# Performance work log

Measured on AMD Instinct MI355X. Metric: run time of the kernel, lower is better.

## Reference

```python
import jax, jax.numpy as jnp
import numpy as np
from jax.scipy.linalg import block_diag

N_STATE, N_INPUT, HORIZON = 32, 16, 64


def setup_inputs() -> dict:
    key = jax.random.key(0)
    kA, kB, kC, kx = jax.random.split(key, 4)
    n_all = N_STATE + N_INPUT
    A = jax.random.normal(kA, (N_STATE, N_STATE), dtype=jnp.float32)
    B = jax.random.normal(kB, (N_STATE, N_INPUT), dtype=jnp.float32)
    Craw = jax.random.normal(kC, (HORIZON, n_all, n_all), dtype=jnp.float32)
    # symmetric positive-definite stage costs -> nonsingular KKT system
    C = jnp.einsum('tij,tkj->tik', Craw, Craw) / jnp.sqrt(jnp.float32(n_all)) \
        + jnp.eye(n_all, dtype=jnp.float32)
    x0 = jax.random.normal(kx, (N_STATE,), dtype=jnp.float32)
    return {"A": A, "B": B, "C": C, "T": HORIZON, "x0": x0}


def reference(A, B, C, T, x0):
    n_state = A.shape[0]
    n_input = B.shape[1]
    n_all = n_state + n_input
    dt = A.dtype

    # cost_mat: block-diagonal [n_all*T, n_all*T]
    cost_mat = block_diag(*C)

    # dynamics: [n_state*T, n_all*T]
    AB = jnp.concatenate((A, B), axis=1)              # [n_state, n_all]
    AB_blk = block_diag(*([AB] * (T - 1)))            # [(T-1)*n_state, (T-1)*n_all]
    dynamics = jnp.zeros((n_state * T, n_all * T), dtype=dt)
    dynamics = dynamics.at[:n_state, :n_state].set(jnp.eye(n_state, dtype=dt))
    dynamics = dynamics.at[n_state:n_state + (T - 1) * n_state,
                           :(T - 1) * n_all].set(AB_blk)
    # -I coupling entries: row n_state*t + i, col n_all*t + i, t=1..T-1
    t = jnp.arange(1, T)
    rows = (n_state * t)[:, None] + jnp.arange(n_state)[None, :]
    cols = (n_all * t)[:, None] + jnp.arange(n_state)[None, :]
    dynamics = dynamics.at[rows, cols].set(jnp.asarray(-1.0, dt))

    zero_mat = jnp.zeros((n_state * T, n_state * T), dtype=dt)
    full_mat = jnp.block([[cost_mat, dynamics.T],
                          [dynamics, zero_mat]])      # [(n_all+n_state)*T]^2

    # rhs: zeros except x0 at the start of the dynamics block
    sol = jnp.zeros(n_all * T + n_state * T, dtype=dt)
    sol = sol.at[n_all * T: n_all * T + n_state].set(x0)

    tau_mu = jnp.linalg.solve(full_mat, sol[:, None])[:, 0]
    tau_star = tau_mu[:n_all * T]
    mu_star = tau_mu[n_all * T:]
    return tau_star, mu_star
```

## Files before the change

kernel.cpp:

```cpp
#include <hip/hip_runtime.h>


namespace {

constexpr int NS  = 32;
constexpr int NI  = 16;
constexpr int NA  = 48;
constexpr int TT  = 64;
constexpr int NTH = 256;

__device__ __forceinline__ void fma4(float4& a, float s, const float4& b) {
  a.x += s * b.x; a.y += s * b.y; a.z += s * b.z; a.w += s * b.w;
}
__device__ __forceinline__ void fms4(float4& a, float s, const float4& b) {
  a.x -= s * b.x; a.y -= s * b.y; a.z -= s * b.z; a.w -= s * b.w;
}
__device__ __forceinline__ float dot4(const float4& a, const float4& b) {
  return a.x * b.x + a.y * b.y + a.z * b.z + a.w * b.w;
}
__device__ __forceinline__ float rdlane(float v, int l) {
  return __int_as_float(__builtin_amdgcn_readlane(__float_as_int(v), l));
}

template<int K>
__device__ __forceinline__ void tile_outer(const float* Acol0, int lda,
                                           const float* Bcol0, int ldb,
                                           float4 acc[4]) {
  #pragma unroll
  for (int m = 0; m < K; ++m) {
    const float4 va = *(const float4*)(Acol0 + m * lda);
    const float4 vb = *(const float4*)(Bcol0 + m * ldb);
    fma4(acc[0], va.x, vb); fma4(acc[1], va.y, vb);
    fma4(acc[2], va.z, vb); fma4(acc[3], va.w, vb);
  }
}

template<int KQ>
__device__ __forceinline__ void tile_dot(const float* Arow0, int lda,
                                         const float* Brow0, int ldb,
                                         float acc[4][4]) {
  #pragma unroll
  for (int q = 0; q < KQ; ++q) {
    float4 va[4], vb[4];
    #pragma unroll
    for (int r = 0; r < 4; ++r) va[r] = *(const float4*)(Arow0 + r * lda + 4 * q);
    #pragma unroll
    for (int c = 0; c < 4; ++c) vb[c] = *(const float4*)(Brow0 + c * ldb + 4 * q);
    #pragma unroll
    for (int r = 0; r < 4; ++r)
      #pragma unroll
      for (int c = 0; c < 4; ++c) acc[r][c] += dot4(va[r], vb[c]);
  }
}

__global__ __launch_bounds__(NTH, 1) void init_elems(
    const float* __restrict__ A, const float* __restrict__ Bm,
    const float* __restrict__ C, float* __restrict__ S0) {
  __shared__ float sC [NA][NA];
  __shared__ float sAB[NS][NA];
  __shared__ float sRi[NI][NI];
  __shared__ float sRiST[NS][NI];
  __shared__ float sBRi [NS][NI];
  const int t = blockIdx.x, tid = threadIdx.x, lane = tid & 63, wid = tid >> 6;
  const float* Ct = C + (size_t)t * NA * NA;

  for (int e = tid; e < NA * NA; e += NTH) sC[e / NA][e % NA] = Ct[e];
  for (int e = tid; e < NS * NA; e += NTH) {
    int i = e / NA, j = e % NA;
    sAB[i][j] = (j < NS) ? A[i * NS + j] : Bm[i * NI + (j - NS)];
  }
  __syncthreads();

  if (wid == 0 && lane < 32) {
    const int c = lane;
    float f[NI];
    #pragma unroll
    for (int i = 0; i < NI; ++i)
      f[i] = (c < NI) ? sC[NS + i][NS + c] : ((c - NI) == i ? 1.f : 0.f);
    #pragma unroll
    for (int k = 0; k < NI; ++k) {
      float mi[NI];
      #pragma unroll
      for (int i = 0; i < NI; ++i) mi[i] = rdlane(f[i], k);
      const float inv = 1.0f / mi[k];
      f[k] *= inv;
      #pragma unroll
      for (int i = 0; i < NI; ++i) if (i != k) f[i] -= mi[i] * f[k];
    }
    if (c >= NI) {
      #pragma unroll
      for (int i = 0; i < NI; ++i) sRi[i][c - NI] = f[i];
    }
  }
  __syncthreads();

  if (tid < 32) {
    const int a = tid >> 2, b = tid & 3;
    float acc[4][4];
    #pragma unroll
    for (int r = 0; r < 4; ++r)
      #pragma unroll
      for (int c = 0; c < 4; ++c) acc[r][c] = 0.f;
    tile_dot<4>(&sC[4 * a][NS], NA, &sRi[4 * b][0], NI, acc);
    #pragma unroll
    for (int r = 0; r < 4; ++r)
      *(float4*)&sRiST[4 * a + r][4 * b] =
          make_float4(acc[r][0], acc[r][1], acc[r][2], acc[r][3]);
  } else if (tid < 64) {
    const int q = tid - 32, a = q >> 2, b = q & 3;
    float acc[4][4];
    #pragma unroll
    for (int r = 0; r < 4; ++r)
      #pragma unroll
      for (int c = 0; c < 4; ++c) acc[r][c] = 0.f;
    tile_dot<4>(&sAB[4 * a][NS], NA, &sRi[4 * b][0], NI, acc);
    #pragma unroll
    for (int r = 0; r < 4; ++r)
      *(float4*)&sBRi[4 * a + r][4 * b] =
          make_float4(acc[r][0], acc[r][1], acc[r][2], acc[r][3]);
  }
  __syncthreads();

  float* outA = S0 + (size_t)t * 3072;
  float* outC = outA + 1024;
  float* outJ = outA + 2048;
  if (tid < 64) {
    const int a = tid >> 3, b = tid & 7;
    float acc[4][4];
    #pragma unroll
    for (int r = 0; r < 4; ++r)
      #pragma unroll
      for (int c = 0; c < 4; ++c) acc[r][c] = 0.f;
    tile_dot<4>(&sRiST[4 * a][0], NI, &sC[4 * b][NS], NA, acc);
    #pragma unroll
    for (int r = 0; r < 4; ++r) {
      const float4 q4 = *(const float4*)&sC[4 * a + r][4 * b];
      *(float4*)(outJ + (4 * a + r) * NS + 4 * b) =
          make_float4(q4.x - acc[r][0], q4.y - acc[r][1],
                      q4.z - acc[r][2], q4.w - acc[r][3]);
    }
  } else if (tid < 128) {
    const int q = tid - 64, a = q >> 3, b = q & 7;
    float acc[4][4];
    #pragma unroll
    for (int r = 0; r < 4; ++r)
      #pragma unroll
      for (int c = 0; c < 4; ++c) acc[r][c] = 0.f;
    tile_dot<4>(&sBRi[4 * a][0], NI, &sC[4 * b][NS], NA, acc);
    #pragma unroll
    for (int r = 0; r < 4; ++r) {
      const float4 a4 = *(const float4*)&sAB[4 * a + r][4 * b];
      *(float4*)(outA + (4 * a + r) * NS + 4 * b) =
          make_float4(a4.x - acc[r][0], a4.y - acc[r][1],
                      a4.z - acc[r][2], a4.w - acc[r][3]);
    }
  } else if (tid < 192) {
    const int q = tid - 128, a = q >> 3, b = q & 7;
    float acc[4][4];
    #pragma unroll
    for (int r = 0; r < 4; ++r)
      #pragma unroll
      for (int c = 0; c < 4; ++c) acc[r][c] = 0.f;
    tile_dot<4>(&sBRi[4 * a][0], NI, &sAB[4 * b][NS], NA, acc);
    #pragma unroll
    for (int r = 0; r < 4; ++r)
      *(float4*)(outC + (4 * a + r) * NS + 4 * b) =
          make_float4(acc[r][0], acc[r][1], acc[r][2], acc[r][3]);
  }
}

__global__ __launch_bounds__(NTH, 1) void scan_level(
    const float* __restrict__ Sin, float* __restrict__ Sout, int off) {
  const int t = blockIdx.x, tid = threadIdx.x, lane = tid & 63, wid = tid >> 6;
  const float* Ei = Sin + (size_t)t * 3072;
  float* Eo = Sout + (size_t)t * 3072;
  if (t + off >= TT) {
    const float4* src = (const float4*)Ei;
    float4* dst = (float4*)Eo;
    #pragma unroll
    for (int r = 0; r < 3; ++r) dst[tid + 256 * r] = src[tid + 256 * r];
    return;
  }
  const float* Ej = Sin + (size_t)(t + off) * 3072;

  __shared__ float sAi[NS][NS], sCi[NS][NS], sJi[NS][NS];
  __shared__ float sAj[NS][NS], sCj[NS][NS], sJj[NS][NS];
  __shared__ float sAjT[NS][NS];
  __shared__ float sT1[NS][NS], sT1T[NS][NS];
  __shared__ float sY1[NS][NS], sY2[NS][NS], sY3T[NS][NS], sW[NS][NS];
  __shared__ float sX[NS][NS], sZ[NS][NS];

  {
    const float4* a4 = (const float4*)Ei;
    ((float4*)sAi)[tid] = a4[tid];
    ((float4*)sCi)[tid] = a4[256 + tid];
    ((float4*)sJi)[tid] = a4[512 + tid];
    const float4* b4 = (const float4*)Ej;
    ((float4*)sAj)[tid] = b4[tid];
    ((float4*)sCj)[tid] = b4[256 + tid];
    ((float4*)sJj)[tid] = b4[512 + tid];
  }
  __syncthreads();
  #pragma unroll
  for (int r = 0; r < 4; ++r) {
    const int e = tid + 256 * r, i = e >> 5, j = e & 31;
    sAjT[j][i] = sAj[i][j];
  }
  if (tid < 64) {
    const int a = tid >> 3, b = tid & 7;
    float4 acc[4] = {make_float4(0,0,0,0), make_float4(0,0,0,0),
                     make_float4(0,0,0,0), make_float4(0,0,0,0)};
    tile_outer<NS>(&sCi[0][4 * a], NS, &sJj[0][4 * b], NS, acc);
    if (a == b) { acc[0].x += 1.f; acc[1].y += 1.f; acc[2].z += 1.f; acc[3].w += 1.f; }
    #pragma unroll
    for (int r = 0; r < 4; ++r) *(float4*)&sX[4 * a + r][4 * b] = acc[r];
  }
  __syncthreads();
  if (wid == 0) {
    const int c = lane;
    float f[NS];
    #pragma unroll
    for (int i = 0; i < NS; ++i)
      f[i] = (c < NS) ? sX[i][c] : ((c - NS) == i ? 1.f : 0.f);
    #pragma unroll
    for (int k = 0; k < NS; ++k) {
      float mi[NS];
      #pragma unroll
      for (int i = 0; i < NS; ++i) mi[i] = rdlane(f[i], k);
      const float inv = 1.0f / mi[k];
      f[k] *= inv;
      #pragma unroll
      for (int i = 0; i < NS; ++i) if (i != k) f[i] -= mi[i] * f[k];
    }
    if (c >= NS) {
      const int col = c - NS;
      #pragma unroll
      for (int i = 0; i < NS; ++i) sT1[i][col] = f[i];
      #pragma unroll
      for (int q = 0; q < 8; ++q)
        *(float4*)&sT1T[col][4 * q] =
            make_float4(f[4 * q], f[4 * q + 1], f[4 * q + 2], f[4 * q + 3]);
    }
  }
  __syncthreads();
  if (tid < 192) {
    const int grp = tid >> 6, q = tid & 63, a = q >> 3, b = q & 7;
    float4 acc[4] = {make_float4(0,0,0,0), make_float4(0,0,0,0),
                     make_float4(0,0,0,0), make_float4(0,0,0,0)};
    if (grp == 0) {
      tile_outer<NS>(&sT1T[0][4 * a], NS, &sAi[0][4 * b], NS, acc);
      #pragma unroll
      for (int r = 0; r < 4; ++r) *(float4*)&sY1[4 * a + r][4 * b] = acc[r];
    } else if (grp == 1) {
      tile_outer<NS>(&sT1T[0][4 * a], NS, &sCi[0][4 * b], NS, acc);
      #pragma unroll
      for (int r = 0; r < 4; ++r) *(float4*)&sY2[4 * a + r][4 * b] = acc[r];
    } else {
      tile_outer<NS>(&sT1[0][4 * a], NS, &sJj[0][4 * b], NS, acc);
      #pragma unroll
      for (int r = 0; r < 4; ++r) *(float4*)&sY3T[4 * a + r][4 * b] = acc[r];
    }
  }
  __syncthreads();
  if (tid < 192) {
    const int grp = tid >> 6, q = tid & 63, a = q >> 3, b = q & 7;
    float4 acc[4] = {make_float4(0,0,0,0), make_float4(0,0,0,0),
                     make_float4(0,0,0,0), make_float4(0,0,0,0)};
    if (grp == 0) {
      tile_outer<NS>(&sAjT[0][4 * a], NS, &sY1[0][4 * b], NS, acc);
      #pragma unroll
      for (int r = 0; r < 4; ++r) *(float4*)&sX[4 * a + r][4 * b] = acc[r];
    } else if (grp == 1) {
      tile_outer<NS>(&sAjT[0][4 * a], NS, &sY2[0][4 * b], NS, acc);
      #pragma unroll
      for (int r = 0; r < 4; ++r) *(float4*)&sZ[4 * a + r][4 * b] = acc[r];
    } else {
      tile_outer<NS>(&sY3T[0][4 * a], NS, &sAi[0][4 * b], NS, acc);
      #pragma unroll
      for (int r = 0; r < 4; ++r) *(float4*)&sW[4 * a + r][4 * b] = acc[r];
    }
  }
  __syncthreads();
  if (tid < 64) {
    const int a = tid >> 3, b = tid & 7;
    float acc[4][4];
    #pragma unroll
    for (int r = 0; r < 4; ++r)
      #pragma unroll
      for (int c = 0; c < 4; ++c) acc[r][c] = 0.f;
    tile_dot<8>(&sZ[4 * a][0], NS, &sAj[4 * b][0], NS, acc);
    #pragma unroll
    for (int r = 0; r < 4; ++r) {
      const float4 c4 = *(const float4*)&sCj[4 * a + r][4 * b];
      *(float4*)&sY2[4 * a + r][4 * b] =
          make_float4(acc[r][0] + c4.x, acc[r][1] + c4.y,
                      acc[r][2] + c4.z, acc[r][3] + c4.w);
    }
  } else if (tid < 128) {
    const int q = tid - 64, a = q >> 3, b = q & 7;
    float4 acc[4] = {make_float4(0,0,0,0), make_float4(0,0,0,0),
                     make_float4(0,0,0,0), make_float4(0,0,0,0)};
    tile_outer<NS>(&sAi[0][4 * a], NS, &sW[0][4 * b], NS, acc);
    #pragma unroll
    for (int r = 0; r < 4; ++r) {
      const float4 j4 = *(const float4*)&sJi[4 * a + r][4 * b];
      acc[r].x += j4.x; acc[r].y += j4.y; acc[r].z += j4.z; acc[r].w += j4.w;
      *(float4*)&sY1[4 * a + r][4 * b] = acc[r];
    }
  }
  __syncthreads();
  {
    float4* o = (float4*)Eo;
    o[tid]       = ((const float4*)sX)[tid];
    o[256 + tid] = ((const float4*)sY2)[tid];
    o[512 + tid] = ((const float4*)sY1)[tid];
  }
}

__global__ __launch_bounds__(NTH, 1) void kmat(
    const float* __restrict__ Sfin, const float* __restrict__ A,
    const float* __restrict__ Bm, const float* __restrict__ C,
    float* __restrict__ Kall, float* __restrict__ Mall) {
  __shared__ float sAB[NS][NA];
  __shared__ float sP [NS][NS];
  __shared__ float sG [NS][NA];
  __shared__ float sFu[NI][NA];
  __shared__ float sK [NI][NS];
  const int t = blockIdx.x, tid = threadIdx.x, lane = tid & 63, wid = tid >> 6;

  for (int e = tid; e < NS * NA; e += NTH) {
    int i = e / NA, j = e % NA;
    sAB[i][j] = (j < NS) ? A[i * NS + j] : Bm[i * NI + (j - NS)];
  }
  if (t == TT - 1) {
    ((float4*)sP)[tid] = make_float4(0.f, 0.f, 0.f, 0.f);
  } else {
    const float4* j4 = (const float4*)(Sfin + (size_t)(t + 1) * 3072 + 2048);
    ((float4*)sP)[tid] = j4[tid];
  }
  const int ui = tid / 12, uk = tid - 12 * ui;
  float4 cr0 = make_float4(0,0,0,0), cr1 = make_float4(0,0,0,0);
  float4 cr2 = make_float4(0,0,0,0), cr3 = make_float4(0,0,0,0);
  if (tid < 48) {
    const float* Ct = C + (size_t)t * NA * NA;
    cr0 = *(const float4*)&Ct[(NS + 4 * ui + 0) * NA + 4 * uk];
    cr1 = *(const float4*)&Ct[(NS + 4 * ui + 1) * NA + 4 * uk];
    cr2 = *(const float4*)&Ct[(NS + 4 * ui + 2) * NA + 4 * uk];
    cr3 = *(const float4*)&Ct[(NS + 4 * ui + 3) * NA + 4 * uk];
  }
  __syncthreads();
  if (tid < 96) {
    const int gi = tid / 12, gk = tid - 12 * gi;
    float4 acc[4] = {make_float4(0,0,0,0), make_float4(0,0,0,0),
                     make_float4(0,0,0,0), make_float4(0,0,0,0)};
    tile_outer<NS>(&sP[0][4 * gi], NS, &sAB[0][4 * gk], NA, acc);
    #pragma unroll
    for (int r = 0; r < 4; ++r) *(float4*)&sG[4 * gi + r][4 * gk] = acc[r];
  }
  __syncthreads();
  if (tid < 48) {
    float4 acc[4] = {cr0, cr1, cr2, cr3};
    tile_outer<NS>(&sAB[0][NS + 4 * ui], NA, &sG[0][4 * uk], NA, acc);
    #pragma unroll
    for (int r = 0; r < 4; ++r) *(float4*)&sFu[4 * ui + r][4 * uk] = acc[r];
  }
  __syncthreads();
  if (wid == 0) {
    const int col = (lane < 16) ? (NS + lane) : (lane - 16);
    float f[NI];
    #pragma unroll
    for (int i = 0; i < NI; ++i) f[i] = sFu[i][col];
    #pragma unroll
    for (int k = 0; k < NI; ++k) {
      float mi[NI];
      #pragma unroll
      for (int i = 0; i < NI; ++i) mi[i] = rdlane(f[i], k);
      const float inv = 1.0f / mi[k];
      f[k] *= inv;
      #pragma unroll
      for (int i = 0; i < NI; ++i) if (i != k) f[i] -= mi[i] * f[k];
    }
    if (lane >= 16 && lane < 48) {
      const int b = lane - 16;
      #pragma unroll
      for (int i = 0; i < NI; ++i) {
        sK[i][b] = f[i];
        Kall[(size_t)t * NI * NS + i * NS + b] = f[i];
      }
    }
  }
  __syncthreads();
  if (tid < 64) {
    const int ma = tid >> 3, mb = tid & 7;
    float4 a0 = *(const float4*)&sAB[4 * ma + 0][4 * mb];
    float4 a1 = *(const float4*)&sAB[4 * ma + 1][4 * mb];
    float4 a2 = *(const float4*)&sAB[4 * ma + 2][4 * mb];
    float4 a3 = *(const float4*)&sAB[4 * ma + 3][4 * mb];
    #pragma unroll
    for (int q = 0; q < 4; ++q) {
      const float4 vf0 = *(const float4*)&sAB[4 * ma + 0][NS + 4 * q];
      const float4 vf1 = *(const float4*)&sAB[4 * ma + 1][NS + 4 * q];
      const float4 vf2 = *(const float4*)&sAB[4 * ma + 2][NS + 4 * q];
      const float4 vf3 = *(const float4*)&sAB[4 * ma + 3][NS + 4 * q];
      #pragma unroll
      for (int d = 0; d < 4; ++d) {
        const float4 vkk = *(const float4*)&sK[4 * q + d][4 * mb];
        const float s0 = (d == 0) ? vf0.x : (d == 1) ? vf0.y : (d == 2) ? vf0.z : vf0.w;
        const float s1 = (d == 0) ? vf1.x : (d == 1) ? vf1.y : (d == 2) ? vf1.z : vf1.w;
        const float s2 = (d == 0) ? vf2.x : (d == 1) ? vf2.y : (d == 2) ? vf2.z : vf2.w;
        const float s3 = (d == 0) ? vf3.x : (d == 1) ? vf3.y : (d == 2) ? vf3.z : vf3.w;
        fms4(a0, s0, vkk); fms4(a1, s1, vkk); fms4(a2, s2, vkk); fms4(a3, s3, vkk);
      }
    }
    float4* Mt = (float4*)(Mall + (size_t)t * NS * NS);
    Mt[(4 * ma + 0) * 8 + mb] = a0;
    Mt[(4 * ma + 1) * 8 + mb] = a1;
    Mt[(4 * ma + 2) * 8 + mb] = a2;
    Mt[(4 * ma + 3) * 8 + mb] = a3;
  }
}

__global__ __launch_bounds__(NTH, 1) void finalize(
    const float* __restrict__ x0, const float* __restrict__ Sfin,
    const float* __restrict__ Kall, const float* __restrict__ Mall,
    float* __restrict__ out) {
  __shared__ float sZx[TT][NS];
  __shared__ float sMb[2 * NS * NS];
  const int tid = threadIdx.x, lane = tid & 63, wid = tid >> 6;

  if (wid == 0) {
    const float4* M4 = (const float4*)Mall;
    float4* sM4 = (float4*)sMb;
    if (lane < NS) { float v = x0[lane]; sZx[0][lane] = v; out[lane] = v; }
    float4 p0 = M4[lane], p1 = M4[64 + lane], p2 = M4[128 + lane], p3 = M4[192 + lane];
    asm volatile("s_waitcnt vmcnt(0)" ::: "memory");
    sM4[lane] = p0; sM4[64 + lane] = p1; sM4[128 + lane] = p2; sM4[192 + lane] = p3;
    asm volatile("s_waitcnt lgkmcnt(0)" ::: "memory");
    __builtin_amdgcn_sched_barrier(0);
    int cur = 0;
    for (int t = 0; t < TT - 1; ++t) {
      const bool pf = (t + 1 < TT - 1);
      if (pf) {
        const int b = (t + 1) * 256;
        p0 = M4[b + lane]; p1 = M4[b + 64 + lane];
        p2 = M4[b + 128 + lane]; p3 = M4[b + 192 + lane];
      }
      if (lane < NS) {
        const float4* xr = (const float4*)&sZx[t][0];
        const float4* mr = sM4 + cur * 256 + 8 * lane;
        float acc = 0.0f;
        #pragma unroll
        for (int q = 0; q < 8; ++q) acc += dot4(mr[q], xr[q]);
        sZx[t + 1][lane] = acc;
        out[(t + 1) * NA + lane] = acc;
      }
      if (pf) {
        asm volatile("s_waitcnt vmcnt(0)" ::: "memory");
        float4* d = sM4 + (cur ^ 1) * 256;
        d[lane] = p0; d[64 + lane] = p1; d[128 + lane] = p2; d[192 + lane] = p3;
      }
      asm volatile("s_waitcnt lgkmcnt(0)" ::: "memory");
      __builtin_amdgcn_sched_barrier(0);
      cur ^= 1;
    }
  }
  __syncthreads();

  const float4* K4 = (const float4*)Kall;
  #pragma unroll
  for (int rep = 0; rep < 4; ++rep) {
    const int idx = tid + 256 * rep;
    const int t = idx >> 4, i = idx & 15;
    const float4* xr = (const float4*)&sZx[t][0];
    float acc = 0.0f;
    #pragma unroll
    for (int q = 0; q < 8; ++q) acc += dot4(K4[(size_t)t * 128 + 8 * i + q], xr[q]);
    out[t * NA + NS + i] = -acc;
  }

  const float4* S4 = (const float4*)Sfin;
  for (int e = tid; e < TT * NS; e += NTH) {
    const int t = e >> 5, i = e & 31;
    const float4* xr = (const float4*)&sZx[t][0];
    float acc = 0.0f;
    #pragma unroll
    for (int q = 0; q < 8; ++q)
      acc += dot4(S4[(size_t)t * 768 + 512 + 8 * i + q], xr[q]);
    out[NA * TT + e] = (t == 0) ? -acc : acc;
  }
}

}

extern "C" void kernel_launch(void* const* d_in, const int* in_sizes, int n_in,
                              void* d_out, int out_size, void* d_ws, size_t ws_size,
                              hipStream_t stream) {
  const float* A  = (const float*)d_in[0];
  const float* Bm = (const float*)d_in[1];
  const float* C  = (const float*)d_in[2];
  const float* x0 = (const float*)d_in[4];
  float* out = (float*)d_out;

  float* Sb0  = (float*)d_ws;
  float* Sb1  = Sb0 + (size_t)TT * 3072;
  float* Kall = Sb1 + (size_t)TT * 3072;
  float* Mall = Kall + (size_t)TT * NI * NS;

  hipLaunchKernelGGL(init_elems, dim3(TT), dim3(NTH), 0, stream, A, Bm, C, Sb0);
  float* bufs[2] = {Sb0, Sb1};
  for (int l = 0; l < 6; ++l) {
    hipLaunchKernelGGL(scan_level, dim3(TT), dim3(NTH), 0, stream,
                       bufs[l & 1], bufs[(l + 1) & 1], 1 << l);
  }
  hipLaunchKernelGGL(kmat, dim3(TT), dim3(NTH), 0, stream,
                     Sb0, A, Bm, C, Kall, Mall);
  hipLaunchKernelGGL(finalize, dim3(1), dim3(NTH), 0, stream,
                     x0, Sb0, Kall, Mall, out);
}
```

Before: 138.0 us.

## Fuse all LQR stages into one persistent kernel with a software grid barrier

Merges the init, six scan levels, gain computation and finalize kernels into a single 64-block persistent kernel. Stages are separated by an atomic-counter grid barrier, which removes per-launch overhead between the many small dependent launches. The forward state rollout appears to be restructured, using cross-lane reads and a shared state buffer in workspace, and output is produced in parallel per block. It relies on all 64 blocks being co-resident and on the spin barrier being correct, and it adds a memset launch to reset the barrier counters.

```diff
diff --git a/kernel.cpp b/kernel.cpp
--- a/kernel.cpp
+++ b/kernel.cpp
@@ -8,6 +8,7 @@
 constexpr int NA  = 48;
 constexpr int TT  = 64;
 constexpr int NTH = 256;
+constexpr int NBLK = 64;
 
 __device__ __forceinline__ void fma4(float4& a, float s, const float4& b) {
   a.x += s * b.x; a.y += s * b.y; a.z += s * b.z; a.w += s * b.w;
@@ -53,440 +54,447 @@
   }
 }
 
-__global__ __launch_bounds__(NTH, 1) void init_elems(
+__device__ __forceinline__ void gbar(unsigned* cnt, unsigned* gen) {
+  __syncthreads();
+  if (threadIdx.x == 0) {
+    __threadfence();
+    const unsigned g = atomicAdd(gen, 0u);
+    const unsigned old = atomicAdd(cnt, 1u);
+    if (old == NBLK - 1) {
+      atomicExch(cnt, 0u);
+      __threadfence();
+      atomicAdd(gen, 1u);
+    } else {
+      while (atomicAdd(gen, 0u) == g) __builtin_amdgcn_s_sleep(2);
+    }
+    __threadfence();
+  }
+  __syncthreads();
+}
+
+__device__ __forceinline__ float step_dot(const float4 m[8], float x) {
+  float a0 = 0.f, a1 = 0.f, a2 = 0.f, a3 = 0.f;
+  #pragma unroll
+  for (int q = 0; q < 8; ++q) {
+    a0 += rdlane(x, 4 * q + 0) * m[q].x;
+    a1 += rdlane(x, 4 * q + 1) * m[q].y;
+    a2 += rdlane(x, 4 * q + 2) * m[q].z;
+    a3 += rdlane(x, 4 * q + 3) * m[q].w;
+  }
+  return (a0 + a1) + (a2 + a3);
+}
+
+__global__ __launch_bounds__(NTH, 1) void lqr_all(
     const float* __restrict__ A, const float* __restrict__ Bm,
-    const float* __restrict__ C, float* __restrict__ S0) {
+    const float* __restrict__ C, const float* __restrict__ x0,
+    float* __restrict__ out,
+    float* __restrict__ Sb0, float* __restrict__ Sb1,
+    float* __restrict__ Kall, float* __restrict__ Mall,
+    float* __restrict__ xs, unsigned* __restrict__ bar) {
   __shared__ float sC [NA][NA];
   __shared__ float sAB[NS][NA];
   __shared__ float sRi[NI][NI];
   __shared__ float sRiST[NS][NI];
   __shared__ float sBRi [NS][NI];
-  const int t = blockIdx.x, tid = threadIdx.x, lane = tid & 63, wid = tid >> 6;
-  const float* Ct = C + (size_t)t * NA * NA;
-
-  for (int e = tid; e < NA * NA; e += NTH) sC[e / NA][e % NA] = Ct[e];
-  for (int e = tid; e < NS * NA; e += NTH) {
-    int i = e / NA, j = e % NA;
-    sAB[i][j] = (j < NS) ? A[i * NS + j] : Bm[i * NI + (j - NS)];
-  }
-  __syncthreads();
-
-  if (wid == 0 && lane < 32) {
-    const int c = lane;
-    float f[NI];
-    #pragma unroll
-    for (int i = 0; i < NI; ++i)
-      f[i] = (c < NI) ? sC[NS + i][NS + c] : ((c - NI) == i ? 1.f : 0.f);
-    #pragma unroll
-    for (int k = 0; k < NI; ++k) {
-      float mi[NI];
-      #pragma unroll
-      for (int i = 0; i < NI; ++i) mi[i] = rdlane(f[i], k);
-      const float inv = 1.0f / mi[k];
-      f[k] *= inv;
-      #pragma unroll
-      for (int i = 0; i < NI; ++i) if (i != k) f[i] -= mi[i] * f[k];
-    }
-    if (c >= NI) {
-      #pragma unroll
-      for (int i = 0; i < NI; ++i) sRi[i][c - NI] = f[i];
-    }
-  }
-  __syncthreads();
-
-  if (tid < 32) {
-    const int a = tid >> 2, b = tid & 3;
-    float acc[4][4];
-    #pragma unroll
-    for (int r = 0; r < 4; ++r)
-      #pragma unroll
-      for (int c = 0; c < 4; ++c) acc[r][c] = 0.f;
-    tile_dot<4>(&sC[4 * a][NS], NA, &sRi[4 * b][0], NI, acc);
-    #pragma unroll
-    for (int r = 0; r < 4; ++r)
-      *(float4*)&sRiST[4 * a + r][4 * b] =
-          make_float4(acc[r][0], acc[r][1], acc[r][2], acc[r][3]);
-  } else if (tid < 64) {
-    const int q = tid - 32, a = q >> 2, b = q & 3;
-    float acc[4][4];
-    #pragma unroll
-    for (int r = 0; r < 4; ++r)
-      #pragma unroll
-      for (int c = 0; c < 4; ++c) acc[r][c] = 0.f;
-    tile_dot<4>(&sAB[4 * a][NS], NA, &sRi[4 * b][0], NI, acc);
-    #pragma unroll
-    for (int r = 0; r < 4; ++r)
-      *(float4*)&sBRi[4 * a + r][4 * b] =
-          make_float4(acc[r][0], acc[r][1], acc[r][2], acc[r][3]);
-  }
-  __syncthreads();
-
-  float* outA = S0 + (size_t)t * 3072;
-  float* outC = outA + 1024;
-  float* outJ = outA + 2048;
-  if (tid < 64) {
-    const int a = tid >> 3, b = tid & 7;
-    float acc[4][4];
-    #pragma unroll
-    for (int r = 0; r < 4; ++r)
-      #pragma unroll
-      for (int c = 0; c < 4; ++c) acc[r][c] = 0.f;
-    tile_dot<4>(&sRiST[4 * a][0], NI, &sC[4 * b][NS], NA, acc);
-    #pragma unroll
-    for (int r = 0; r < 4; ++r) {
-      const float4 q4 = *(const float4*)&sC[4 * a + r][4 * b];
-      *(float4*)(outJ + (4 * a + r) * NS + 4 * b) =
-          make_float4(q4.x - acc[r][0], q4.y - acc[r][1],
-                      q4.z - acc[r][2], q4.w - acc[r][3]);
-    }
-  } else if (tid < 128) {
-    const int q = tid - 64, a = q >> 3, b = q & 7;
-    float acc[4][4];
-    #pragma unroll
-    for (int r = 0; r < 4; ++r)
-      #pragma unroll
-      for (int c = 0; c < 4; ++c) acc[r][c] = 0.f;
-    tile_dot<4>(&sBRi[4 * a][0], NI, &sC[4 * b][NS], NA, acc);
-    #pragma unroll
-    for (int r = 0; r < 4; ++r) {
-      const float4 a4 = *(const float4*)&sAB[4 * a + r][4 * b];
-      *(float4*)(outA + (4 * a + r) * NS + 4 * b) =
-          make_float4(a4.x - acc[r][0], a4.y - acc[r][1],
-                      a4.z - acc[r][2], a4.w - acc[r][3]);
-    }
-  } else if (tid < 192) {
-    const int q = tid - 128, a = q >> 3, b = q & 7;
-    float acc[4][4];
-    #pragma unroll
-    for (int r = 0; r < 4; ++r)
-      #pragma unroll
-      for (int c = 0; c < 4; ++c) acc[r][c] = 0.f;
-    tile_dot<4>(&sBRi[4 * a][0], NI, &sAB[4 * b][NS], NA, acc);
-    #pragma unroll
-    for (int r = 0; r < 4; ++r)
-      *(float4*)(outC + (4 * a + r) * NS + 4 * b) =
-          make_float4(acc[r][0], acc[r][1], acc[r][2], acc[r][3]);
-  }
-}
-
-__global__ __launch_bounds__(NTH, 1) void scan_level(
-    const float* __restrict__ Sin, float* __restrict__ Sout, int off) {
-  const int t = blockIdx.x, tid = threadIdx.x, lane = tid & 63, wid = tid >> 6;
-  const float* Ei = Sin + (size_t)t * 3072;
-  float* Eo = Sout + (size_t)t * 3072;
-  if (t + off >= TT) {
-    const float4* src = (const float4*)Ei;
-    float4* dst = (float4*)Eo;
-    #pragma unroll
-    for (int r = 0; r < 3; ++r) dst[tid + 256 * r] = src[tid + 256 * r];
-    return;
-  }
-  const float* Ej = Sin + (size_t)(t + off) * 3072;
-
   __shared__ float sAi[NS][NS], sCi[NS][NS], sJi[NS][NS];
-  __shared__ float sAj[NS][NS], sCj[NS][NS], sJj[NS][NS];
-  __shared__ float sAjT[NS][NS];
+  __shared__ float sAj[NS][NS], sCj[NS][NS], sJj[NS][NS], sAjT[NS][NS];
   __shared__ float sT1[NS][NS], sT1T[NS][NS];
   __shared__ float sY1[NS][NS], sY2[NS][NS], sY3T[NS][NS], sW[NS][NS];
-  __shared__ float sX[NS][NS], sZ[NS][NS];
+  __shared__ float sX[NS][NS], sZm[NS][NS];
+  __shared__ float sP[NS][NS], sG[NS][NA], sFu[NI][NA], sK[NI][NS];
+
+  const int t = blockIdx.x, tid = threadIdx.x, lane = tid & 63, wid = tid >> 6;
+  unsigned* cnt = bar;
+  unsigned* gen = bar + 1;
 
   {
-    const float4* a4 = (const float4*)Ei;
-    ((float4*)sAi)[tid] = a4[tid];
-    ((float4*)sCi)[tid] = a4[256 + tid];
-    ((float4*)sJi)[tid] = a4[512 + tid];
-    const float4* b4 = (const float4*)Ej;
-    ((float4*)sAj)[tid] = b4[tid];
-    ((float4*)sCj)[tid] = b4[256 + tid];
-    ((float4*)sJj)[tid] = b4[512 + tid];
-  }
-  __syncthreads();
-  #pragma unroll
-  for (int r = 0; r < 4; ++r) {
-    const int e = tid + 256 * r, i = e >> 5, j = e & 31;
-    sAjT[j][i] = sAj[i][j];
-  }
-  if (tid < 64) {
-    const int a = tid >> 3, b = tid & 7;
-    float4 acc[4] = {make_float4(0,0,0,0), make_float4(0,0,0,0),
-                     make_float4(0,0,0,0), make_float4(0,0,0,0)};
-    tile_outer<NS>(&sCi[0][4 * a], NS, &sJj[0][4 * b], NS, acc);
-    if (a == b) { acc[0].x += 1.f; acc[1].y += 1.f; acc[2].z += 1.f; acc[3].w += 1.f; }
-    #pragma unroll
-    for (int r = 0; r < 4; ++r) *(float4*)&sX[4 * a + r][4 * b] = acc[r];
-  }
-  __syncthreads();
-  if (wid == 0) {
-    const int c = lane;
-    float f[NS];
-    #pragma unroll
-    for (int i = 0; i < NS; ++i)
-      f[i] = (c < NS) ? sX[i][c] : ((c - NS) == i ? 1.f : 0.f);
-    #pragma unroll
-    for (int k = 0; k < NS; ++k) {
-      float mi[NS];
-      #pragma unroll
-      for (int i = 0; i < NS; ++i) mi[i] = rdlane(f[i], k);
-      const float inv = 1.0f / mi[k];
-      f[k] *= inv;
-      #pragma unroll
-      for (int i = 0; i < NS; ++i) if (i != k) f[i] -= mi[i] * f[k];
-    }
-    if (c >= NS) {
-      const int col = c - NS;
-      #pragma unroll
-      for (int i = 0; i < NS; ++i) sT1[i][col] = f[i];
-      #pragma unroll
-      for (int q = 0; q < 8; ++q)
-        *(float4*)&sT1T[col][4 * q] =
-            make_float4(f[4 * q], f[4 * q + 1], f[4 * q + 2], f[4 * q + 3]);
-    }
-  }
-  __syncthreads();
-  if (tid < 192) {
-    const int grp = tid >> 6, q = tid & 63, a = q >> 3, b = q & 7;
-    float4 acc[4] = {make_float4(0,0,0,0), make_float4(0,0,0,0),
-                     make_float4(0,0,0,0), make_float4(0,0,0,0)};
-    if (grp == 0) {
-      tile_outer<NS>(&sT1T[0][4 * a], NS, &sAi[0][4 * b], NS, acc);
-      #pragma unroll
-      for (int r = 0; r < 4; ++r) *(float4*)&sY1[4 * a + r][4 * b] = acc[r];
-    } else if (grp == 1) {
-      tile_outer<NS>(&sT1T[0][4 * a], NS, &sCi[0][4 * b], NS, acc);
-      #pragma unroll
-      for (int r = 0; r < 4; ++r) *(float4*)&sY2[4 * a + r][4 * b] = acc[r];
+    const float* Ct = C + (size_t)t * NA * NA;
+    for (int e = tid; e < NA * NA; e += NTH) sC[e / NA][e % NA] = Ct[e];
+    for (int e = tid; e < NS * NA; e += NTH) {
+      int i = e / NA, j = e % NA;
+      sAB[i][j] = (j < NS) ? A[i * NS + j] : Bm[i * NI + (j - NS)];
+    }
+    __syncthreads();
+    if (wid == 0 && lane < 32) {
+      const int c = lane;
+      float f[NI];
+      #pragma unroll
+      for (int i = 0; i < NI; ++i)
+        f[i] = (c < NI) ? sC[NS + i][NS + c] : ((c - NI) == i ? 1.f : 0.f);
+      #pragma unroll
+      for (int k = 0; k < NI; ++k) {
+        float mi[NI];
+        #pragma unroll
+        for (int i = 0; i < NI; ++i) mi[i] = rdlane(f[i], k);
+        const float inv = 1.0f / mi[k];
+        f[k] *= inv;
+        #pragma unroll
+        for (int i = 0; i < NI; ++i) if (i != k) f[i] -= mi[i] * f[k];
+      }
+      if (c >= NI) {
+        #pragma unroll
+        for (int i = 0; i < NI; ++i) sRi[i][c - NI] = f[i];
+      }
+    }
+    __syncthreads();
+    if (tid < 32) {
+      const int a = tid >> 2, b = tid & 3;
+      float acc[4][4];
+      #pragma unroll
+      for (int r = 0; r < 4; ++r)
+        #pragma unroll
+        for (int c = 0; c < 4; ++c) acc[r][c] = 0.f;
+      tile_dot<4>(&sC[4 * a][NS], NA, &sRi[4 * b][0], NI, acc);
+      #pragma unroll
+      for (int r = 0; r < 4; ++r)
+        *(float4*)&sRiST[4 * a + r][4 * b] =
+            make_float4(acc[r][0], acc[r][1], acc[r][2], acc[r][3]);
+    } else if (tid < 64) {
+      const int q = tid - 32, a = q >> 2, b = q & 3;
+      float acc[4][4];
+      #pragma unroll
+      for (int r = 0; r < 4; ++r)
+        #pragma unroll
+        for (int c = 0; c < 4; ++c) acc[r][c] = 0.f;
+      tile_dot<4>(&sAB[4 * a][NS], NA, &sRi[4 * b][0], NI, acc);
+      #pragma unroll
+      for (int r = 0; r < 4; ++r)
+        *(float4*)&sBRi[4 * a + r][4 * b] =
+            make_float4(acc[r][0], acc[r][1], acc[r][2], acc[r][3]);
+    }
+    __syncthreads();
+    float* outA = Sb0 + (size_t)t * 3072;
+    float* outC = outA + 1024;
+    float* outJ = outA + 2048;
+    if (tid < 64) {
+      const int a = tid >> 3, b = tid & 7;
+      float acc[4][4];
+      #pragma unroll
+      for (int r = 0; r < 4; ++r)
+        #pragma unroll
+        for (int c = 0; c < 4; ++c) acc[r][c] = 0.f;
+      tile_dot<4>(&sRiST[4 * a][0], NI, &sC[4 * b][NS], NA, acc);
+      #pragma unroll
+      for (int r = 0; r < 4; ++r) {
+        const float4 q4 = *(const float4*)&sC[4 * a + r][4 * b];
+        *(float4*)(outJ + (4 * a + r) * NS + 4 * b) =
+            make_float4(q4.x - acc[r][0], q4.y - acc[r][1],
+                        q4.z - acc[r][2], q4.w - acc[r][3]);
+      }
+    } else if (tid < 128) {
+      const int q = tid - 64, a = q >> 3, b = q & 7;
+      float acc[4][4];
+      #pragma unroll
+      for (int r = 0; r < 4; ++r)
+        #pragma unroll
+        for (int c = 0; c < 4; ++c) acc[r][c] = 0.f;
+      tile_dot<4>(&sBRi[4 * a][0], NI, &sC[4 * b][NS], NA, acc);
+      #pragma unroll
+      for (int r = 0; r < 4; ++r) {
+        const float4 a4 = *(const float4*)&sAB[4 * a + r][4 * b];
+        *(float4*)(outA + (4 * a + r) * NS + 4 * b) =
+            make_float4(a4.x - acc[r][0], a4.y - acc[r][1],
+                        a4.z - acc[r][2], a4.w - acc[r][3]);
+      }
+    } else if (tid < 192) {
+      const int q = tid - 128, a = q >> 3, b = q & 7;
+      float acc[4][4];
+      #pragma unroll
+      for (int r = 0; r < 4; ++r)
+        #pragma unroll
+        for (int c = 0; c < 4; ++c) acc[r][c] = 0.f;
+      tile_dot<4>(&sBRi[4 * a][0], NI, &sAB[4 * b][NS], NA, acc);
+      #pragma unroll
+      for (int r = 0; r < 4; ++r)
+        *(float4*)(outC + (4 * a + r) * NS + 4 * b) =
+            make_float4(acc[r][0], acc[r][1], acc[r][2], acc[r][3]);
+    }
+  }
+  gbar(cnt, gen);
+
+  for (int l = 0; l < 6; ++l) {
+    const int off = 1 << l;
+    const float* Sin = (l & 1) ? Sb1 : Sb0;
+    float* Sout = (l & 1) ? Sb0 : Sb1;
+    const float* Ei = Sin + (size_t)t * 3072;
+    float* Eo = Sout + (size_t)t * 3072;
+    if (t + off >= TT) {
+      const float4* src = (const float4*)Ei;
+      float4* dst = (float4*)Eo;
+      #pragma unroll
+      for (int r = 0; r < 3; ++r) dst[tid + 256 * r] = src[tid + 256 * r];
     } else {
-      tile_outer<NS>(&sT1[0][4 * a], NS, &sJj[0][4 * b], NS, acc);
-      #pragma unroll
-      for (int r = 0; r < 4; ++r) *(float4*)&sY3T[4 * a + r][4 * b] = acc[r];
-    }
-  }
-  __syncthreads();
-  if (tid < 192) {
-    const int grp = tid >> 6, q = tid & 63, a = q >> 3, b = q & 7;
-    float4 acc[4] = {make_float4(0,0,0,0), make_float4(0,0,0,0),
-                     make_float4(0,0,0,0), make_float4(0,0,0,0)};
-    if (grp == 0) {
-      tile_outer<NS>(&sAjT[0][4 * a], NS, &sY1[0][4 * b], NS, acc);
-      #pragma unroll
-      for (int r = 0; r < 4; ++r) *(float4*)&sX[4 * a + r][4 * b] = acc[r];
-    } else if (grp == 1) {
-      tile_outer<NS>(&sAjT[0][4 * a], NS, &sY2[0][4 * b], NS, acc);
-      #pragma unroll
-      for (int r = 0; r < 4; ++r) *(float4*)&sZ[4 * a + r][4 * b] = acc[r];
+      const float* Ej = Sin + (size_t)(t + off) * 3072;
+      {
+        const float4* a4 = (const float4*)Ei;
+        ((float4*)sAi)[tid] = a4[tid];
+        ((float4*)sCi)[tid] = a4[256 + tid];
+        ((float4*)sJi)[tid] = a4[512 + tid];
+        const float4* b4 = (const float4*)Ej;
+        ((float4*)sAj)[tid] = b4[tid];
+        ((float4*)sCj)[tid] = b4[256 + tid];
+        ((float4*)sJj)[tid] = b4[512 + tid];
+      }
+      __syncthreads();
+      #pragma unroll
+      for (int r = 0; r < 4; ++r) {
+        const int e = tid + 256 * r, i = e >> 5, j = e & 31;
+        sAjT[j][i] = sAj[i][j];
+      }
+      if (tid < 64) {
+        const int a = tid >> 3, b = tid & 7;
+        float4 acc[4] = {make_float4(0,0,0,0), make_float4(0,0,0,0),
+                         make_float4(0,0,0,0), make_float4(0,0,0,0)};
+        tile_outer<NS>(&sCi[0][4 * a], NS, &sJj[0][4 * b], NS, acc);
+        if (a == b) { acc[0].x += 1.f; acc[1].y += 1.f; acc[2].z += 1.f; acc[3].w += 1.f; }
+        #pragma unroll
+        for (int r = 0; r < 4; ++r) *(float4*)&sX[4 * a + r][4 * b] = acc[r];
+      }
+      __syncthreads();
+      if (wid == 0) {
+        const int c = lane;
+        float f[NS];
+        #pragma unroll
+        for (int i = 0; i < NS; ++i)
+          f[i] = (c < NS) ? sX[i][c] : ((c - NS) == i ? 1.f : 0.f);
+        #pragma unroll
+        for (int k = 0; k < NS; ++k) {
+          float mi[NS];
+          #pragma unroll
+          for (int i = 0; i < NS; ++i) mi[i] = rdlane(f[i], k);
+          const float inv = 1.0f / mi[k];
+          f[k] *= inv;
+          #pragma unroll
+          for (int i = 0; i < NS; ++i) if (i != k) f[i] -= mi[i] * f[k];
+        }
+        if (c >= NS) {
+          const int col = c - NS;
+          #pragma unroll
+          for (int i = 0; i < NS; ++i) sT1[i][col] = f[i];
+          #pragma unroll
+          for (int q = 0; q < 8; ++q)
+            *(float4*)&sT1T[col][4 * q] =
+                make_float4(f[4 * q], f[4 * q + 1], f[4 * q + 2], f[4 * q + 3]);
+        }
+      }
+      __syncthreads();
+      if (tid < 192) {
+        const int grp = tid >> 6, q = tid & 63, a = q >> 3, b = q & 7;
+        float4 acc[4] = {make_float4(0,0,0,0), make_float4(0,0,0,0),
+                         make_float4(0,0,0,0), make_float4(0,0,0,0)};
+        if (grp == 0) {
+          tile_outer<NS>(&sT1T[0][4 * a], NS, &sAi[0][4 * b], NS, acc);
+          #pragma unroll
+          for (int r = 0; r < 4; ++r) *(float4*)&sY1[4 * a + r][4 * b] = acc[r];
+        } else if (grp == 1) {
+          tile_outer<NS>(&sT1T[0][4 * a], NS, &sCi[0][4 * b], NS, acc);
+          #pragma unroll
+          for (int r = 0; r < 4; ++r) *(float4*)&sY2[4 * a + r][4 * b] = acc[r];
+        } else {
+          tile_outer<NS>(&sT1[0][4 * a], NS, &sJj[0][4 * b], NS, acc);
+          #pragma unroll
+          for (int r = 0; r < 4; ++r) *(float4*)&sY3T[4 * a + r][4 * b] = acc[r];
+        }
+      }
+      __syncthreads();
+      if (tid < 192) {
+        const int grp = tid >> 6, q = tid & 63, a = q >> 3, b = q & 7;
+        float4 acc[4] = {make_float4(0,0,0,0), make_float4(0,0,0,0),
+                         make_float4(0,0,0,0), make_float4(0,0,0,0)};
+        if (grp == 0) {
+          tile_outer<NS>(&sAjT[0][4 * a], NS, &sY1[0][4 * b], NS, acc);
+          #pragma unroll
+          for (int r = 0; r < 4; ++r) *(float4*)&sX[4 * a + r][4 * b] = acc[r];
+        } else if (grp == 1) {
+          tile_outer<NS>(&sAjT[0][4 * a], NS, &sY2[0][4 * b], NS, acc);
+          #pragma unroll
+          for (int r = 0; r < 4; ++r) *(float4*)&sZm[4 * a + r][4 * b] = acc[r];
+        } else {
+          tile_outer<NS>(&sY3T[0][4 * a], NS, &sAi[0][4 * b], NS, acc);
+          #pragma unroll
+          for (int r = 0; r < 4; ++r) *(float4*)&sW[4 * a + r][4 * b] = acc[r];
+        }
+      }
+      __syncthreads();
+      if (tid < 64) {
+        const int a = tid >> 3, b = tid & 7;
+        float acc[4][4];
+        #pragma unroll
+        for (int r = 0; r < 4; ++r)
+          #pragma unroll
+          for (int c = 0; c < 4; ++c) acc[r][c] = 0.f;
+        tile_dot<8>(&sZm[4 * a][0], NS, &sAj[4 * b][0], NS, acc);
+        #pragma unroll
+        for (int r = 0; r < 4; ++r) {
+          const float4 c4 = *(const float4*)&sCj[4 * a + r][4 * b];
+          *(float4*)&sY2[4 * a + r][4 * b] =
+              make_float4(acc[r][0] + c4.x, acc[r][1] + c4.y,
+                          acc[r][2] + c4.z, acc[r][3] + c4.w);
+        }
+      } else if (tid < 128) {
+        const int q = tid - 64, a = q >> 3, b = q & 7;
+        float4 acc[4] = {make_float4(0,0,0,0), make_float4(0,0,0,0),
+                         make_float4(0,0,0,0), make_float4(0,0,0,0)};
+        tile_outer<NS>(&sAi[0][4 * a], NS, &sW[0][4 * b], NS, acc);
+        #pragma unroll
+        for (int r = 0; r < 4; ++r) {
+          const float4 j4 = *(const float4*)&sJi[4 * a + r][4 * b];
+          acc[r].x += j4.x; acc[r].y += j4.y; acc[r].z += j4.z; acc[r].w += j4.w;
+          *(float4*)&sY1[4 * a + r][4 * b] = acc[r];
+        }
+      }
+      __syncthreads();
+      {
+        float4* o = (float4*)Eo;
+        o[tid]       = ((const float4*)sX)[tid];
+        o[256 + tid] = ((const float4*)sY2)[tid];
+        o[512 + tid] = ((const float4*)sY1)[tid];
+      }
+    }
+    gbar(cnt, gen);
+  }
+
+  {
+    for (int e = tid; e < NS * NA; e += NTH) {
+      int i = e / NA, j = e % NA;
+      sAB[i][j] = (j < NS) ? A[i * NS + j] : Bm[i * NI + (j - NS)];
+    }
+    if (t == TT - 1) {
+      ((float4*)sP)[tid] = make_float4(0.f, 0.f, 0.f, 0.f);
     } else {
-      tile_outer<NS>(&sY3T[0][4 * a], NS, &sAi[0][4 * b], NS, acc);
-      #pragma unroll
-      for (int r = 0; r < 4; ++r) *(float4*)&sW[4 * a + r][4 * b] = acc[r];
-    }
-  }
-  __syncthreads();
-  if (tid < 64) {
-    const int a = tid >> 3, b = tid & 7;
-    float acc[4][4];
-    #pragma unroll
-    for (int r = 0; r < 4; ++r)
-      #pragma unroll
-      for (int c = 0; c < 4; ++c) acc[r][c] = 0.f;
-    tile_dot<8>(&sZ[4 * a][0], NS, &sAj[4 * b][0], NS, acc);
-    #pragma unroll
-    for (int r = 0; r < 4; ++r) {
-      const float4 c4 = *(const float4*)&sCj[4 * a + r][4 * b];
-      *(float4*)&sY2[4 * a + r][4 * b] =
-          make_float4(acc[r][0] + c4.x, acc[r][1] + c4.y,
-                      acc[r][2] + c4.z, acc[r][3] + c4.w);
-    }
-  } else if (tid < 128) {
-    const int q = tid - 64, a = q >> 3, b = q & 7;
-    float4 acc[4] = {make_float4(0,0,0,0), make_float4(0,0,0,0),
-                     make_float4(0,0,0,0), make_float4(0,0,0,0)};
-    tile_outer<NS>(&sAi[0][4 * a], NS, &sW[0][4 * b], NS, acc);
-    #pragma unroll
-    for (int r = 0; r < 4; ++r) {
-      const float4 j4 = *(const float4*)&sJi[4 * a + r][4 * b];
-      acc[r].x += j4.x; acc[r].y += j4.y; acc[r].z += j4.z; acc[r].w += j4.w;
-      *(float4*)&sY1[4 * a + r][4 * b] = acc[r];
-    }
-  }
-  __syncthreads();
+      const float4* j4 = (const float4*)(Sb0 + (size_t)(t + 1) * 3072 + 2048);
+      ((float4*)sP)[tid] = j4[tid];
+    }
+    const int ui = tid / 12, uk = tid - 12 * ui;
+    float4 cr0 = make_float4(0,0,0,0), cr1 = make_float4(0,0,0,0);
+    float4 cr2 = make_float4(0,0,0,0), cr3 = make_float4(0,0,0,0);
+    if (tid < 48) {
+      const float* Ct = C + (size_t)t * NA * NA;
+      cr0 = *(const float4*)&Ct[(NS + 4 * ui + 0) * NA + 4 * uk];
+      cr1 = *(const float4*)&Ct[(NS + 4 * ui + 1) * NA + 4 * uk];
+      cr2 = *(const float4*)&Ct[(NS + 4 * ui + 2) * NA + 4 * uk];
+      cr3 = *(const float4*)&Ct[(NS + 4 * ui + 3) * NA + 4 * uk];
+    }
+    __syncthreads();
+    if (tid < 96) {
+      const int gi = tid / 12, gk = tid - 12 * gi;
+      float4 acc[4] = {make_float4(0,0,0,0), make_float4(0,0,0,0),
+                       make_float4(0,0,0,0), make_float4(0,0,0,0)};
+      tile_outer<NS>(&sP[0][4 * gi], NS, &sAB[0][4 * gk], NA, acc);
+      #pragma unroll
+      for (int r = 0; r < 4; ++r) *(float4*)&sG[4 * gi + r][4 * gk] = acc[r];
+    }
+    __syncthreads();
+    if (tid < 48) {
+      float4 acc[4] = {cr0, cr1, cr2, cr3};
+      tile_outer<NS>(&sAB[0][NS + 4 * ui], NA, &sG[0][4 * uk], NA, acc);
+      #pragma unroll
+      for (int r = 0; r < 4; ++r) *(float4*)&sFu[4 * ui + r][4 * uk] = acc[r];
+    }
+    __syncthreads();
+    if (wid == 0) {
+      const int col = (lane < 16) ? (NS + lane) : (lane - 16);
+      float f[NI];
+      #pragma unroll
+      for (int i = 0; i < NI; ++i) f[i] = sFu[i][col];
+      #pragma unroll
+      for (int k = 0; k < NI; ++k) {
+        float mi[NI];
+        #pragma unroll
+        for (int i = 0; i < NI; ++i) mi[i] = rdlane(f[i], k);
+        const float inv = 1.0f / mi[k];
+        f[k] *= inv;
+        #pragma unroll
+        for (int i = 0; i < NI; ++i) if (i != k) f[i] -= mi[i] * f[k];
+      }
+      if (lane >= 16 && lane < 48) {
+        const int b = lane - 16;
+        #pragma unroll
+        for (int i = 0; i < NI; ++i) {
+          sK[i][b] = f[i];
+          Kall[(size_t)t * NI * NS + i * NS + b] = f[i];
+        }
+      }
+    }
+    __syncthreads();
+    if (tid < 64) {
+      const int ma = tid >> 3, mb = tid & 7;
+      float4 a0 = *(const float4*)&sAB[4 * ma + 0][4 * mb];
+      float4 a1 = *(const float4*)&sAB[4 * ma + 1][4 * mb];
+      float4 a2 = *(const float4*)&sAB[4 * ma + 2][4 * mb];
+      float4 a3 = *(const float4*)&sAB[4 * ma + 3][4 * mb];
+      #pragma unroll
+      for (int q = 0; q < 4; ++q) {
+        const float4 vf0 = *(const float4*)&sAB[4 * ma + 0][NS + 4 * q];
+        const float4 vf1 = *(const float4*)&sAB[4 * ma + 1][NS + 4 * q];
+        const float4 vf2 = *(const float4*)&sAB[4 * ma + 2][NS + 4 * q];
+        const float4 vf3 = *(const float4*)&sAB[4 * ma + 3][NS + 4 * q];
+        #pragma unroll
+        for (int d = 0; d < 4; ++d) {
+          const float4 vkk = *(const float4*)&sK[4 * q + d][4 * mb];
+          const float s0 = (d == 0) ? vf0.x : (d == 1) ? vf0.y : (d == 2) ? vf0.z : vf0.w;
+          const float s1 = (d == 0) ? vf1.x : (d == 1) ? vf1.y : (d == 2) ? vf1.z : vf1.w;
+          const float s2 = (d == 0) ? vf2.x : (d == 1) ? vf2.y : (d == 2) ? vf2.z : vf2.w;
+          const float s3 = (d == 0) ? vf3.x : (d == 1) ? vf3.y : (d == 2) ? vf3.z : vf3.w;
+          fms4(a0, s0, vkk); fms4(a1, s1, vkk); fms4(a2, s2, vkk); fms4(a3, s3, vkk);
+        }
+      }
+      float4* Mt = (float4*)(Mall + (size_t)t * NS * NS);
+      Mt[(4 * ma + 0) * 8 + mb] = a0;
+      Mt[(4 * ma + 1) * 8 + mb] = a1;
+      Mt[(4 * ma + 2) * 8 + mb] = a2;
+      Mt[(4 * ma + 3) * 8 + mb] = a3;
+    }
+  }
+  gbar(cnt, gen);
+
+  if (t == 0 && wid == 0) {
+    const int i = lane;
+    if (i < NS) {
+      const float4* Mg = (const float4*)Mall;
+      float4 mA[8], mB[8];
+      float x = x0[i];
+      out[i] = x; xs[i] = x;
+      #pragma unroll
+      for (int q = 0; q < 8; ++q) mA[q] = Mg[0 * 256 + i * 8 + q];
+      #pragma unroll
+      for (int q = 0; q < 8; ++q) mB[q] = Mg[1 * 256 + i * 8 + q];
+      for (int s = 0; s < TT - 1; s += 2) {
+        x = step_dot(mA, x);
+        out[(s + 1) * NA + i] = x; xs[(s + 1) * NS + i] = x;
+        if (s + 2 < TT - 1) {
+          #pragma unroll
+          for (int q = 0; q < 8; ++q) mA[q] = Mg[(s + 2) * 256 + i * 8 + q];
+        }
+        if (s + 1 < TT - 1) {
+          x = step_dot(mB, x);
+          out[(s + 2) * NA + i] = x; xs[(s + 2) * NS + i] = x;
+          if (s + 3 < TT - 1) {
+            #pragma unroll
+            for (int q = 0; q < 8; ++q) mB[q] = Mg[(s + 3) * 256 + i * 8 + q];
+          }
+        }
+      }
+    }
+  }
+  gbar(cnt, gen);
+
   {
-    float4* o = (float4*)Eo;
-    o[tid]       = ((const float4*)sX)[tid];
-    o[256 + tid] = ((const float4*)sY2)[tid];
-    o[512 + tid] = ((const float4*)sY1)[tid];
-  }
-}
-
-__global__ __launch_bounds__(NTH, 1) void kmat(
-    const float* __restrict__ Sfin, const float* __restrict__ A,
-    const float* __restrict__ Bm, const float* __restrict__ C,
-    float* __restrict__ Kall, float* __restrict__ Mall) {
-  __shared__ float sAB[NS][NA];
-  __shared__ float sP [NS][NS];
-  __shared__ float sG [NS][NA];
-  __shared__ float sFu[NI][NA];
-  __shared__ float sK [NI][NS];
-  const int t = blockIdx.x, tid = threadIdx.x, lane = tid & 63, wid = tid >> 6;
-
-  for (int e = tid; e < NS * NA; e += NTH) {
-    int i = e / NA, j = e % NA;
-    sAB[i][j] = (j < NS) ? A[i * NS + j] : Bm[i * NI + (j - NS)];
-  }
-  if (t == TT - 1) {
-    ((float4*)sP)[tid] = make_float4(0.f, 0.f, 0.f, 0.f);
-  } else {
-    const float4* j4 = (const float4*)(Sfin + (size_t)(t + 1) * 3072 + 2048);
-    ((float4*)sP)[tid] = j4[tid];
-  }
-  const int ui = tid / 12, uk = tid - 12 * ui;
-  float4 cr0 = make_float4(0,0,0,0), cr1 = make_float4(0,0,0,0);
-  float4 cr2 = make_float4(0,0,0,0), cr3 = make_float4(0,0,0,0);
-  if (tid < 48) {
-    const float* Ct = C + (size_t)t * NA * NA;
-    cr0 = *(const float4*)&Ct[(NS + 4 * ui + 0) * NA + 4 * uk];
-    cr1 = *(const float4*)&Ct[(NS + 4 * ui + 1) * NA + 4 * uk];
-    cr2 = *(const float4*)&Ct[(NS + 4 * ui + 2) * NA + 4 * uk];
-    cr3 = *(const float4*)&Ct[(NS + 4 * ui + 3) * NA + 4 * uk];
-  }
-  __syncthreads();
-  if (tid < 96) {
-    const int gi = tid / 12, gk = tid - 12 * gi;
-    float4 acc[4] = {make_float4(0,0,0,0), make_float4(0,0,0,0),
-                     make_float4(0,0,0,0), make_float4(0,0,0,0)};
-    tile_outer<NS>(&sP[0][4 * gi], NS, &sAB[0][4 * gk], NA, acc);
-    #pragma unroll
-    for (int r = 0; r < 4; ++r) *(float4*)&sG[4 * gi + r][4 * gk] = acc[r];
-  }
-  __syncthreads();
-  if (tid < 48) {
-    float4 acc[4] = {cr0, cr1, cr2, cr3};
-    tile_outer<NS>(&sAB[0][NS + 4 * ui], NA, &sG[0][4 * uk], NA, acc);
-    #pragma unroll
-    for (int r = 0; r < 4; ++r) *(float4*)&sFu[4 * ui + r][4 * uk] = acc[r];
-  }
-  __syncthreads();
-  if (wid == 0) {
-    const int col = (lane < 16) ? (NS + lane) : (lane - 16);
-    float f[NI];
-    #pragma unroll
-    for (int i = 0; i < NI; ++i) f[i] = sFu[i][col];
-    #pragma unroll
-    for (int k = 0; k < NI; ++k) {
-      float mi[NI];
-      #pragma unroll
-      for (int i = 0; i < NI; ++i) mi[i] = rdlane(f[i], k);
-      const float inv = 1.0f / mi[k];
-      f[k] *= inv;
-      #pragma unroll
-      for (int i = 0; i < NI; ++i) if (i != k) f[i] -= mi[i] * f[k];
-    }
-    if (lane >= 16 && lane < 48) {
-      const int b = lane - 16;
-      #pragma unroll
-      for (int i = 0; i < NI; ++i) {
-        sK[i][b] = f[i];
-        Kall[(size_t)t * NI * NS + i * NS + b] = f[i];
-      }
-    }
-  }
-  __syncthreads();
-  if (tid < 64) {
-    const int ma = tid >> 3, mb = tid & 7;
-    float4 a0 = *(const float4*)&sAB[4 * ma + 0][4 * mb];
-    float4 a1 = *(const float4*)&sAB[4 * ma + 1][4 * mb];
-    float4 a2 = *(const float4*)&sAB[4 * ma + 2][4 * mb];
-    float4 a3 = *(const float4*)&sAB[4 * ma + 3][4 * mb];
-    #pragma unroll
-    for (int q = 0; q < 4; ++q) {
-      const float4 vf0 = *(const float4*)&sAB[4 * ma + 0][NS + 4 * q];
-      const float4 vf1 = *(const float4*)&sAB[4 * ma + 1][NS + 4 * q];
-      const float4 vf2 = *(const float4*)&sAB[4 * ma + 2][NS + 4 * q];
-      const float4 vf3 = *(const float4*)&sAB[4 * ma + 3][NS + 4 * q];
-      #pragma unroll
-      for (int d = 0; d < 4; ++d) {
-        const float4 vkk = *(const float4*)&sK[4 * q + d][4 * mb];
-        const float s0 = (d == 0) ? vf0.x : (d == 1) ? vf0.y : (d == 2) ? vf0.z : vf0.w;
-        const float s1 = (d == 0) ? vf1.x : (d == 1) ? vf1.y : (d == 2) ? vf1.z : vf1.w;
-        const float s2 = (d == 0) ? vf2.x : (d == 1) ? vf2.y : (d == 2) ? vf2.z : vf2.w;
-        const float s3 = (d == 0) ? vf3.x : (d == 1) ? vf3.y : (d == 2) ? vf3.z : vf3.w;
-        fms4(a0, s0, vkk); fms4(a1, s1, vkk); fms4(a2, s2, vkk); fms4(a3, s3, vkk);
-      }
-    }
-    float4* Mt = (float4*)(Mall + (size_t)t * NS * NS);
-    Mt[(4 * ma + 0) * 8 + mb] = a0;
-    Mt[(4 * ma + 1) * 8 + mb] = a1;
-    Mt[(4 * ma + 2) * 8 + mb] = a2;
-    Mt[(4 * ma + 3) * 8 + mb] = a3;
-  }
-}
-
-__global__ __launch_bounds__(NTH, 1) void finalize(
-    const float* __restrict__ x0, const float* __restrict__ Sfin,
-    const float* __restrict__ Kall, const float* __restrict__ Mall,
-    float* __restrict__ out) {
-  __shared__ float sZx[TT][NS];
-  __shared__ float sMb[2 * NS * NS];
-  const int tid = threadIdx.x, lane = tid & 63, wid = tid >> 6;
-
-  if (wid == 0) {
-    const float4* M4 = (const float4*)Mall;
-    float4* sM4 = (float4*)sMb;
-    if (lane < NS) { float v = x0[lane]; sZx[0][lane] = v; out[lane] = v; }
-    float4 p0 = M4[lane], p1 = M4[64 + lane], p2 = M4[128 + lane], p3 = M4[192 + lane];
-    asm volatile("s_waitcnt vmcnt(0)" ::: "memory");
-    sM4[lane] = p0; sM4[64 + lane] = p1; sM4[128 + lane] = p2; sM4[192 + lane] = p3;
-    asm volatile("s_waitcnt lgkmcnt(0)" ::: "memory");
-    __builtin_amdgcn_sched_barrier(0);
-    int cur = 0;
-    for (int t = 0; t < TT - 1; ++t) {
-      const bool pf = (t + 1 < TT - 1);
-      if (pf) {
-        const int b = (t + 1) * 256;
-        p0 = M4[b + lane]; p1 = M4[b + 64 + lane];
-        p2 = M4[b + 128 + lane]; p3 = M4[b + 192 + lane];
-      }
-      if (lane < NS) {
-        const float4* xr = (const float4*)&sZx[t][0];
-        const float4* mr = sM4 + cur * 256 + 8 * lane;
-        float acc = 0.0f;
-        #pragma unroll
-        for (int q = 0; q < 8; ++q) acc += dot4(mr[q], xr[q]);
-        sZx[t + 1][lane] = acc;
-        out[(t + 1) * NA + lane] = acc;
-      }
-      if (pf) {
-        asm volatile("s_waitcnt vmcnt(0)" ::: "memory");
-        float4* d = sM4 + (cur ^ 1) * 256;
-        d[lane] = p0; d[64 + lane] = p1; d[128 + lane] = p2; d[192 + lane] = p3;
-      }
-      asm volatile("s_waitcnt lgkmcnt(0)" ::: "memory");
-      __builtin_amdgcn_sched_barrier(0);
-      cur ^= 1;
-    }
-  }
-  __syncthreads();
-
-  const float4* K4 = (const float4*)Kall;
-  #pragma unroll
-  for (int rep = 0; rep < 4; ++rep) {
-    const int idx = tid + 256 * rep;
-    const int t = idx >> 4, i = idx & 15;
-    const float4* xr = (const float4*)&sZx[t][0];
-    float acc = 0.0f;
-    #pragma unroll
-    for (int q = 0; q < 8; ++q) acc += dot4(K4[(size_t)t * 128 + 8 * i + q], xr[q]);
-    out[t * NA + NS + i] = -acc;
-  }
-
-  const float4* S4 = (const float4*)Sfin;
-  for (int e = tid; e < TT * NS; e += NTH) {
-    const int t = e >> 5, i = e & 31;
-    const float4* xr = (const float4*)&sZx[t][0];
-    float acc = 0.0f;
-    #pragma unroll
-    for (int q = 0; q < 8; ++q)
-      acc += dot4(S4[(size_t)t * 768 + 512 + 8 * i + q], xr[q]);
-    out[NA * TT + e] = (t == 0) ? -acc : acc;
+    const float4* xr = (const float4*)(xs + (size_t)t * NS);
+    if (tid < NI) {
+      const float4* Kr = (const float4*)(Kall + (size_t)t * NI * NS + tid * NS);
+      float acc = 0.f;
+      #pragma unroll
+      for (int q = 0; q < 8; ++q) acc += dot4(Kr[q], xr[q]);
+      out[t * NA + NS + tid] = -acc;
+    } else if (tid < NI + NS) {
+      const int i = tid - NI;
+      const float4* Pr = (const float4*)(Sb0 + (size_t)t * 3072 + 2048 + i * NS);
+      float acc = 0.f;
+      #pragma unroll
+      for (int q = 0; q < 8; ++q) acc += dot4(Pr[q], xr[q]);
+      out[NA * TT + t * NS + i] = (t == 0) ? -acc : acc;
+    }
   }
 }
 
@@ -505,15 +513,10 @@
   float* Sb1  = Sb0 + (size_t)TT * 3072;
   float* Kall = Sb1 + (size_t)TT * 3072;
   float* Mall = Kall + (size_t)TT * NI * NS;
-
-  hipLaunchKernelGGL(init_elems, dim3(TT), dim3(NTH), 0, stream, A, Bm, C, Sb0);
-  float* bufs[2] = {Sb0, Sb1};
-  for (int l = 0; l < 6; ++l) {
-    hipLaunchKernelGGL(scan_level, dim3(TT), dim3(NTH), 0, stream,
-                       bufs[l & 1], bufs[(l + 1) & 1], 1 << l);
-  }
-  hipLaunchKernelGGL(kmat, dim3(TT), dim3(NTH), 0, stream,
-                     Sb0, A, Bm, C, Kall, Mall);
-  hipLaunchKernelGGL(finalize, dim3(1), dim3(NTH), 0, stream,
-                     x0, Sb0, Kall, Mall, out);
-}
+  float* xs   = Mall + (size_t)TT * NS * NS;
+  unsigned* bar = (unsigned*)(xs + (size_t)TT * NS);
+
+  hipMemsetAsync(bar, 0, 8 * sizeof(unsigned), stream);
+  hipLaunchKernelGGL(lqr_all, dim3(NBLK), dim3(NTH), 0, stream,
+                     A, Bm, C, x0, out, Sb0, Sb1, Kall, Mall, xs, bar);
+}
```

Result: slower. 185.9 us (+34.7%).
